# Performance work log

Measured on AMD Instinct MI355X. Metric: run time of the kernel, lower is better.

Reference implementation:

```python
import jax, jax.numpy as jnp
import numpy as np

N, E, G = 51200, 819200, 256            # nodes, directed edges, graphs
N2, A, E2 = 102400, 204800, 409600      # 2-sets, assignments, 2-set edges
D, L, NI2, NAF = 64, 5, 36, 40          # emb_dim, num_layer, num_i_2, num_atom_features
EPS = 1e-5


def _seg_sum(v, seg, n):
    return jax.ops.segment_sum(v, seg, num_segments=n)


def _seg_mean(v, seg, n):
    s = jax.ops.segment_sum(v, seg, num_segments=n)
    c = jax.ops.segment_sum(jnp.ones((v.shape[0],), v.dtype), seg, num_segments=n)
    return s / jnp.maximum(c, 1.0)[:, None]


def setup_inputs() -> dict:
    key = jax.random.key(0)
    ks = iter(jax.random.split(key, 64))
    nrm = lambda shape: jax.random.normal(next(ks), shape, jnp.float32) * 0.1
    x = jax.random.normal(next(ks), (N, NAF), jnp.float32)
    edge_index = jax.random.randint(next(ks), (2, E), 0, N, dtype=jnp.int32)
    edge_attr = jnp.stack([jax.random.randint(next(ks), (E,), 0, 4, dtype=jnp.int32),
                           jax.random.randint(next(ks), (E,), 0, 3, dtype=jnp.int32)], axis=1)
    batch = jnp.repeat(jnp.arange(G, dtype=jnp.int32), N // G)
    iso_type_2 = jax.nn.one_hot(jax.random.randint(next(ks), (N2,), 0, NI2), NI2, dtype=jnp.float32)
    edge_index_2 = jax.random.randint(next(ks), (2, E2), 0, N2, dtype=jnp.int32)
    assignment_index_2 = jnp.stack([jax.random.randint(next(ks), (A,), 0, N, dtype=jnp.int32),
                                    jnp.repeat(jnp.arange(N2, dtype=jnp.int32), 2)], axis=0)
    batch_2 = jnp.repeat(jnp.arange(G, dtype=jnp.int32), N2 // G)
    params = dict(
        emb_W=nrm((NAF, D)), emb_b=jnp.zeros((D,), jnp.float32),
        gin_W1=nrm((L, D, 2 * D)), gin_b1=jnp.zeros((L, 2 * D), jnp.float32),
        gin_W2=nrm((L, 2 * D, D)), gin_b2=jnp.zeros((L, D), jnp.float32),
        eemb1=nrm((L, 6, D)), eemb2=nrm((L, 3, D)),
        bn_gamma=jnp.ones((L, D), jnp.float32), bn_beta=jnp.zeros((L, D), jnp.float32),
        iso1_rel_W=nrm((D + NI2, D)), iso1_rel_b=jnp.zeros((D,), jnp.float32),
        iso1_root_W=nrm((D + NI2, D)),
        iso2_rel_W=nrm((D, D)), iso2_rel_b=jnp.zeros((D,), jnp.float32),
        iso2_root_W=nrm((D, D)),
        ro_W0=nrm((2 * D, D)), ro_b0=jnp.zeros((D,), jnp.float32),
        ro_W1=nrm((D, D // 2)), ro_b1=jnp.zeros((D // 2,), jnp.float32),
        ro_W2=nrm((D // 2, D // 4)), ro_b2=jnp.zeros((D // 4,), jnp.float32),
        last_W=nrm((D // 4, 1)), last_b=jnp.zeros((1,), jnp.float32),
    )
    return dict(x=x, edge_index=edge_index, edge_attr=edge_attr, batch=batch,
                iso_type_2=iso_type_2, edge_index_2=edge_index_2,
                assignment_index_2=assignment_index_2, batch_2=batch_2, **params)


def _forward(x, iso_type_2, emb_W, emb_b, gin_W1, gin_b1, gin_W2, gin_b2,
             eemb1, eemb2, bn_gamma, bn_beta,
             iso1_rel_W, iso1_rel_b, iso1_root_W, iso2_rel_W, iso2_rel_b, iso2_root_W,
             ro_W0, ro_b0, ro_W1, ro_b1, ro_W2, ro_b2, last_W, last_b,
             edge_index, edge_attr, batch, edge_index_2, assignment_index_2, batch_2):
    # --- GIN stack with edge-feature embeddings and self loops ---
    loop = jnp.arange(N, dtype=edge_index.dtype)
    src = jnp.concatenate([edge_index[0], loop])
    dst = jnp.concatenate([edge_index[1], loop])
    sl_attr = jnp.tile(jnp.array([[4, 0]], dtype=edge_attr.dtype), (N, 1))
    ea = jnp.concatenate([edge_attr, sl_attr], axis=0)  # [E+N, 2]

    h = jax.nn.relu(x @ emb_W + emb_b)  # x_embedding1
    for l in range(L):
        e = eemb1[l][ea[:, 0]] + eemb2[l][ea[:, 1]]      # [E+N, D]
        agg = _seg_sum(h[src] + e, dst, N)               # gather + scatter-add
        h2 = jax.nn.relu(agg @ gin_W1[l] + gin_b1[l]) @ gin_W2[l] + gin_b2[l]
        mu = jnp.mean(h2, axis=0)
        var = jnp.var(h2, axis=0)                        # biased, torch BN training mode
        h2 = (h2 - mu) / jnp.sqrt(var + EPS) * bn_gamma[l] + bn_beta[l]
        h = h2 if l == L - 1 else jax.nn.relu(h2)        # last layer: no ReLU (JK='last')
    node_rep = h

    # --- graph mean pool of node representation ---
    x1 = _seg_mean(node_rep, batch, G)                   # [G, D]

    # --- 2-set branch: avg_pool onto 2-sets, concat iso type, two GraphConvs ---
    xp = _seg_mean(node_rep[assignment_index_2[0]], assignment_index_2[1], N2)
    xp = jnp.concatenate([xp, iso_type_2], axis=1)       # [N2, D+NI2]

    def graph_conv(z, Wrel, brel, Wroot):
        agg = _seg_sum(z[edge_index_2[0]], edge_index_2[1], N2)
        return agg @ Wrel + brel + z @ Wroot

    xp = jax.nn.relu(graph_conv(xp, iso1_rel_W, iso1_rel_b, iso1_root_W))
    xp = jax.nn.relu(graph_conv(xp, iso2_rel_W, iso2_rel_b, iso2_root_W))
    x2 = _seg_mean(xp, batch_2, G)                       # [G, D]

    # --- readout MLP ---
    m = jnp.concatenate([x1, x2], axis=1)                # [G, 2D]
    m = jax.nn.relu(m @ ro_W0 + ro_b0)
    m = jax.nn.relu(m @ ro_W1 + ro_b1)
    m = jax.nn.relu(m @ ro_W2 + ro_b2)
    m = m @ last_W + last_b
    return m.reshape(-1)                                 # num_tasks == 1 -> flat [G]


def reference(x, edge_index, edge_attr, batch, iso_type_2, edge_index_2,
              assignment_index_2, batch_2, emb_W, emb_b, gin_W1, gin_b1, gin_W2,
              gin_b2, eemb1, eemb2, bn_gamma, bn_beta, iso1_rel_W, iso1_rel_b,
              iso1_root_W, iso2_rel_W, iso2_rel_b, iso2_root_W, ro_W0, ro_b0,
              ro_W1, ro_b1, ro_W2, ro_b2, last_W, last_b):
    return _forward(x, iso_type_2, emb_W, emb_b, gin_W1, gin_b1, gin_W2, gin_b2,
                    eemb1, eemb2, bn_gamma, bn_beta,
                    iso1_rel_W, iso1_rel_b, iso1_root_W, iso2_rel_W, iso2_rel_b,
                    iso2_root_W, ro_W0, ro_b0, ro_W1, ro_b1, ro_W2, ro_b2,
                    last_W, last_b, edge_index, edge_attr, batch, edge_index_2,
                    assignment_index_2, batch_2)
```

## Files before the change

kernel.cpp:

```cpp
#include <hip/hip_runtime.h>

#define NN   51200
#define EE   819200
#define GG   256
#define NN2  102400
#define AA   204800
#define EE2  409600
#define DD   64
#define LL   5

typedef __attribute__((ext_vector_type(8))) short bf16x8;
typedef __attribute__((ext_vector_type(4))) float f32x4;
typedef unsigned short ushort_t;

#define OFF_H      ((size_t)0)
#define OFF_AGG    ((size_t)13107200)
#define OFF_H2     ((size_t)26214400)
#define OFF_XP     ((size_t)39321600)
#define OFF_PERM   ((size_t)60293120)
#define OFF_YROOT  ((size_t)65536000)
#define OFF_OFFS1  ((size_t)91750400)
#define OFF_COL1   ((size_t)91955216)
#define OFF_OFFS2  ((size_t)95232016)
#define OFF_COL2   ((size_t)95641632)
#define OFF_CNT1   ((size_t)97280032)
#define OFF_CUR1   ((size_t)97484832)
#define OFF_CNT2   ((size_t)97689632)
#define OFF_CUR2   ((size_t)98099232)
#define OFF_STATS  ((size_t)98508832)
#define ZERO_BYTES ((size_t)1231360)
#define OFF_ISO    ((size_t)98511392)
#define OFF_M      ((size_t)98920992)
#define WS_NEEDED  ((size_t)99052064)

__device__ __forceinline__ int waveInclScan(int v, int lane) {
#pragma unroll
    for (int off = 1; off < 64; off <<= 1) {
        int t = __shfl_up(v, off, 64);
        if (lane >= off) v += t;
    }
    return v;
}

__device__ __forceinline__ void bsplit(float x, ushort_t& hi, ushort_t& lo) {
    union { float f; unsigned u; } a; a.f = x;
    unsigned hb = (a.u + 0x7FFFu + ((a.u >> 16) & 1u)) >> 16;
    union { unsigned u; float f; } h; h.u = hb << 16;
    float r = x - h.f;
    union { float f; unsigned u; } b; b.f = r;
    unsigned lb = (b.u + 0x7FFFu + ((b.u >> 16) & 1u)) >> 16;
    hi = (ushort_t)hb; lo = (ushort_t)lb;
}

__global__ void khist_m(const int* __restrict__ dst1, const int* __restrict__ dst2,
                        int* __restrict__ cnt1, int* __restrict__ cnt2,
                        int* __restrict__ rank1, int* __restrict__ rank2) {
    int b = blockIdx.x;
    if (b < 800) {
        int i = (b * 256 + threadIdx.x) * 4;
        int4 d = *(const int4*)(dst1 + i);
        int4 r;
        r.x = atomicAdd(&cnt1[d.x], 1);
        r.y = atomicAdd(&cnt1[d.y], 1);
        r.z = atomicAdd(&cnt1[d.z], 1);
        r.w = atomicAdd(&cnt1[d.w], 1);
        *(int4*)(rank1 + i) = r;
    } else {
        int i = ((b - 800) * 256 + threadIdx.x) * 4;
        int4 d = *(const int4*)(dst2 + i);
        int4 r;
        r.x = atomicAdd(&cnt2[d.x], 1);
        r.y = atomicAdd(&cnt2[d.y], 1);
        r.z = atomicAdd(&cnt2[d.z], 1);
        r.w = atomicAdd(&cnt2[d.w], 1);
        *(int4*)(rank2 + i) = r;
    }
}

__global__ void kprepx(const float* __restrict__ x, const float* __restrict__ embW,
                       const float* __restrict__ embB, float* __restrict__ h,
                       const float* __restrict__ gW1, const float* __restrict__ gW2,
                       ushort_t* __restrict__ w1h, ushort_t* __restrict__ w1l,
                       ushort_t* __restrict__ w2h, ushort_t* __restrict__ w2l,
                       const float* __restrict__ iso, int* __restrict__ isoIdx) {
    int b = blockIdx.x;
    if (b < 12800) {
        int t = b * 256 + threadIdx.x;
        int n = t >> 6, d = t & 63;
        float acc = embB[d];
        const float* xr = x + n * 40;
#pragma unroll
        for (int k = 0; k < 40; ++k) acc = fmaf(xr[k], embW[k * 64 + d], acc);
        h[(size_t)n * 64 + d] = fmaxf(acc, 0.f);
    } else if (b < 12840) {
        int t = (b - 12800) * 256 + threadIdx.x;
        int lane = t & 63, frag = t >> 6;
        int c15 = lane & 15, q = lane >> 4;
        if (frag < 80) {
            int kt = frag & 1, nt = (frag >> 1) & 7, l = frag >> 4;
            const float* W = gW1 + l * 8192;
            ushort_t* oh = w1h + ((size_t)frag * 64 + lane) * 8;
            ushort_t* ol = w1l + ((size_t)frag * 64 + lane) * 8;
            int kb = kt * 32 + q * 8, colw = nt * 16 + c15;
#pragma unroll
            for (int j = 0; j < 8; ++j) {
                ushort_t hi, lo; bsplit(W[(kb + j) * 128 + colw], hi, lo);
                oh[j] = hi; ol[j] = lo;
            }
        } else if (frag < 160) {
            int f = frag - 80;
            int kt = f & 3, nt = (f >> 2) & 3, l = f >> 4;
            const float* W = gW2 + l * 8192;
            ushort_t* oh = w2h + ((size_t)f * 64 + lane) * 8;
            ushort_t* ol = w2l + ((size_t)f * 64 + lane) * 8;
            int kb = kt * 32 + q * 8, colw = nt * 16 + c15;
#pragma unroll
            for (int j = 0; j < 8; ++j) {
                ushort_t hi, lo; bsplit(W[(kb + j) * 64 + colw], hi, lo);
                oh[j] = hi; ol[j] = lo;
            }
        }
    } else {
        int j = (b - 12840) * 256 + threadIdx.x;
        const float4* r4 = (const float4*)(iso + (size_t)j * 36);
        int best = 0;
#pragma unroll
        for (int k = 0; k < 9; ++k) {
            float4 v = r4[k];
            if (v.x > 0.5f) best = 4 * k;
            if (v.y > 0.5f) best = 4 * k + 1;
            if (v.z > 0.5f) best = 4 * k + 2;
            if (v.w > 0.5f) best = 4 * k + 3;
        }
        isoIdx[j] = best;
    }
}

__global__ void kreduce_m(const int* __restrict__ cnt1, const int* __restrict__ cnt2,
                          int* __restrict__ bsum1, int* __restrict__ bsum2) {
    __shared__ int wsr[4];
    int b = blockIdx.x;
    const int* cnt; int* bsum;
    if (b < 50) { cnt = cnt1; bsum = bsum1; }
    else { b -= 50; cnt = cnt2; bsum = bsum2; }
    int tid = threadIdx.x, lane = tid & 63, wid = tid >> 6;
    int4 v = ((const int4*)(cnt + (size_t)b * 1024))[tid];
    int s = v.x + v.y + v.z + v.w;
#pragma unroll
    for (int off = 32; off; off >>= 1) s += __shfl_down(s, off, 64);
    if (lane == 0) wsr[wid] = s;
    __syncthreads();
    if (tid == 0) bsum[b] = wsr[0] + wsr[1] + wsr[2] + wsr[3];
}

__global__ void kscan_small_m(const int* __restrict__ bsum1, const int* __restrict__ bsum2,
                              int* __restrict__ boffs1, int* __restrict__ boffs2) {
    __shared__ int w0s;
    const int* bsum = blockIdx.x ? bsum2 : bsum1;
    int* boffs = blockIdx.x ? boffs2 : boffs1;
    int nb = blockIdx.x ? 100 : 50;
    int tid = threadIdx.x, lane = tid & 63, wid = tid >> 6;
    int v = (tid < nb) ? bsum[tid] : 0;
    int incl = waveInclScan(v, lane);
    if (tid == 63) w0s = incl;
    __syncthreads();
    int excl = incl - v + (wid ? w0s : 0);
    if (tid < nb) boffs[tid] = excl;
}

__global__ void kscan_apply_m(const int* __restrict__ cnt1, const int* __restrict__ cnt2,
                              const int* __restrict__ boffs1, const int* __restrict__ boffs2,
                              int* __restrict__ offs1, int* __restrict__ offs2,
                              int* __restrict__ dbin) {
    __shared__ int wsum[4];
    __shared__ int hbin[64];
    int b = blockIdx.x;
    const int* cnt; const int* boffs; int* offs; int n, total;
    bool g1 = (b < 50);
    if (g1) { cnt = cnt1; boffs = boffs1; offs = offs1; n = NN; total = EE; }
    else { b -= 50; cnt = cnt2; boffs = boffs2; offs = offs2; n = NN2; total = EE2; }
    int tid = threadIdx.x, lane = tid & 63, wid = tid >> 6;
    if (g1 && tid < 64) hbin[tid] = 0;
    size_t base = (size_t)b * 1024;
    int4 v = ((const int4*)(cnt + base))[tid];
    int s = v.x + v.y + v.z + v.w;
    int incl = waveInclScan(s, lane);
    if (lane == 63) wsum[wid] = incl;
    __syncthreads();
    if (g1) {
        atomicAdd(&hbin[v.x < 63 ? v.x : 63], 1);
        atomicAdd(&hbin[v.y < 63 ? v.y : 63], 1);
        atomicAdd(&hbin[v.z < 63 ? v.z : 63], 1);
        atomicAdd(&hbin[v.w < 63 ? v.w : 63], 1);
    }
    int woff = boffs[b];
#pragma unroll
    for (int w = 0; w < 3; ++w) woff += (w < wid) ? wsum[w] : 0;
    int excl = woff + incl - s;
    int4 o;
    o.x = excl; o.y = excl + v.x; o.z = o.y + v.y; o.w = o.z + v.z;
    ((int4*)(offs + base))[tid] = o;
    if (tid == 0 && b == 0) offs[n] = total;
    __syncthreads();
    if (g1 && tid < 64 && hbin[tid]) atomicAdd(&dbin[tid], hbin[tid]);
}

__global__ void kdegscan(const int* __restrict__ dbin, int* __restrict__ dstart) {
    int tid = threadIdx.x;
    int v = dbin[tid];
    int incl = waveInclScan(v, tid);
    dstart[tid] = NN - incl;
}

__global__ __launch_bounds__(256) void kfill2(
        const int* __restrict__ src1, const int* __restrict__ dst1,
        const int* __restrict__ ea, const int* __restrict__ rank1,
        const int* __restrict__ offs1, int* __restrict__ col1,
        const int* __restrict__ src2, const int* __restrict__ dst2,
        const int* __restrict__ rank2, const int* __restrict__ offs2,
        int* __restrict__ col2,
        const int* __restrict__ dstart, int* __restrict__ dcur,
        int* __restrict__ perm) {
    int b = blockIdx.x;
    if (b < 800) {
        int i = (b * 256 + threadIdx.x) * 4;
        int4 d4 = *(const int4*)(dst1 + i);
        int4 s4 = *(const int4*)(src1 + i);
        int4 r4 = *(const int4*)(rank1 + i);
        int4 e0 = *(const int4*)(ea + 2 * i);
        int4 e1 = *(const int4*)(ea + 2 * i + 4);
        col1[offs1[d4.x] + r4.x] = s4.x | ((e0.x * 3 + e0.y) << 16);
        col1[offs1[d4.y] + r4.y] = s4.y | ((e0.z * 3 + e0.w) << 16);
        col1[offs1[d4.z] + r4.z] = s4.z | ((e1.x * 3 + e1.y) << 16);
        col1[offs1[d4.w] + r4.w] = s4.w | ((e1.z * 3 + e1.w) << 16);
    } else if (b < 1200) {
        int i = ((b - 800) * 256 + threadIdx.x) * 4;
        int4 d4 = *(const int4*)(dst2 + i);
        int4 s4 = *(const int4*)(src2 + i);
        int4 r4 = *(const int4*)(rank2 + i);
        col2[offs2[d4.x] + r4.x] = s4.x;
        col2[offs2[d4.y] + r4.y] = s4.y;
        col2[offs2[d4.z] + r4.z] = s4.z;
        col2[offs2[d4.w] + r4.w] = s4.w;
    } else {
        __shared__ int lhist[64];
        __shared__ int lbase[64];
        int tid = threadIdx.x;
        if (tid < 64) lhist[tid] = 0;
        __syncthreads();
        int n = (b - 1200) * 256 + tid;
        int d = offs1[n + 1] - offs1[n]; d = d < 63 ? d : 63;
        int lr = atomicAdd(&lhist[d], 1);
        __syncthreads();
        if (tid < 64) {
            int c = lhist[tid];
            lbase[tid] = c ? atomicAdd(&dcur[tid], c) : 0;
        }
        __syncthreads();
        perm[dstart[d] + lbase[d] + lr] = n;
    }
}

__global__ __launch_bounds__(256) void ktrans(float* __restrict__ h,
                                              const float* __restrict__ pst,
                                              const float* __restrict__ gamma,
                                              const float* __restrict__ beta) {
    __shared__ float sstat[128];
    __shared__ float sSC[64], sSH[64];
    int tid = threadIdx.x;
    if (tid < 128) {
        float s = 0.f;
        const float* p = pst + tid;
#pragma unroll
        for (int i = 0; i < 32; ++i) s += p[i * 128];
        sstat[tid] = s;
    }
    __syncthreads();
    if (tid < 64) {
        float mu = sstat[tid] * (1.f / NN);
        float var = sstat[64 + tid] * (1.f / NN) - mu * mu;
        float sc = gamma[tid] * rsqrtf(var + 1e-5f);
        sSC[tid] = sc; sSH[tid] = beta[tid] - mu * sc;
    }
    __syncthreads();
    int c = (tid & 15) * 4;
    float4 sc4 = *(const float4*)(sSC + c);
    float4 sh4 = *(const float4*)(sSH + c);
    float4* hp = (float4*)h;
    size_t base = (size_t)blockIdx.x * 1024 + tid;
#pragma unroll
    for (int r = 0; r < 4; ++r) {
        float4 v = hp[base + r * 256];
        v.x = fmaxf(fmaf(v.x, sc4.x, sh4.x), 0.f);
        v.y = fmaxf(fmaf(v.y, sc4.y, sh4.y), 0.f);
        v.z = fmaxf(fmaf(v.z, sc4.z, sh4.z), 0.f);
        v.w = fmaxf(fmaf(v.w, sc4.w, sh4.w), 0.f);
        hp[base + r * 256] = v;
    }
}

__global__ __launch_bounds__(256) void kglayer(
    const float* __restrict__ hin, float* __restrict__ hout,
    const int* __restrict__ perm,
    const int* __restrict__ offs, const int* __restrict__ col,
    const float* __restrict__ e1, const float* __restrict__ e2,
    const ushort_t* __restrict__ w1h, const ushort_t* __restrict__ w1l,
    const ushort_t* __restrict__ w2h, const ushort_t* __restrict__ w2l,
    const float* __restrict__ b1, const float* __restrict__ b2,
    float* __restrict__ pstout) {
    __shared__ float etab[13 * 64];
    __shared__ int sPerm[16];
    __shared__ float sMLP[16 * 132];
    float* sA = sMLP;
    float* sH = sMLP;
    int tid = threadIdx.x;
    if (tid < 16) sPerm[tid] = perm[blockIdx.x * 16 + tid];
    for (int idx = tid; idx < 13 * 64; idx += 256) {
        int ci = idx >> 6, dd = idx & 63;
        etab[idx] = e1[(ci / 3) * 64 + dd] + e2[(ci % 3) * 64 + dd];
    }
    __syncthreads();
    int lane = tid & 63, wv = tid >> 6;
    int c15 = lane & 15, q = lane >> 4;

    {
        int n = sPerm[wv * 4 + q];
        int s0 = offs[n], s1 = offs[n + 1];
        float4 sx = *(const float4*)(hin + (size_t)n * 64 + 4 * c15);
        float4 et = *(const float4*)(etab + 12 * 64 + 4 * c15);
        float a0 = sx.x + et.x, a1 = sx.y + et.y, a2 = sx.z + et.z, a3 = sx.w + et.w;
        int deg = s1 - s0;
        if (deg > 0) {
            const int* cp = col + s0;
            int nfull = deg >> 3, rem = deg & 7;
            int vv[8];
#pragma unroll
            for (int j = 0; j < 8; ++j) {
                int idx = j < deg ? j : deg - 1;
                vv[j] = cp[idx];
            }
            for (int it = 0; it < nfull; ++it) {
                float4 xv[8], tv[8];
#pragma unroll
                for (int j = 0; j < 8; ++j) {
                    xv[j] = *(const float4*)(hin + (size_t)(vv[j] & 0xFFFF) * 64 + 4 * c15);
                    tv[j] = *(const float4*)(etab + (vv[j] >> 16) * 64 + 4 * c15);
                }
                int e8 = (it + 1) * 8;
                bool more = e8 < deg;
                int nx[8];
                if (more) {
#pragma unroll
                    for (int j = 0; j < 8; ++j) {
                        int idx = e8 + j; idx = idx < deg ? idx : deg - 1;
                        nx[j] = cp[idx];
                    }
                }
#pragma unroll
                for (int j = 0; j < 8; ++j) {
                    a0 += xv[j].x + tv[j].x;
                    a1 += xv[j].y + tv[j].y;
                    a2 += xv[j].z + tv[j].z;
                    a3 += xv[j].w + tv[j].w;
                }
                if (more) {
#pragma unroll
                    for (int j = 0; j < 8; ++j) vv[j] = nx[j];
                }
            }
            if (rem) {
                float4 xv[8], tv[8];
#pragma unroll
                for (int j = 0; j < 8; ++j) {
                    xv[j] = *(const float4*)(hin + (size_t)(vv[j] & 0xFFFF) * 64 + 4 * c15);
                    tv[j] = *(const float4*)(etab + (vv[j] >> 16) * 64 + 4 * c15);
                }
#pragma unroll
                for (int j = 0; j < 8; ++j) {
                    float mm = (j < rem) ? 1.f : 0.f;
                    a0 = fmaf(xv[j].x + tv[j].x, mm, a0);
                    a1 = fmaf(xv[j].y + tv[j].y, mm, a1);
                    a2 = fmaf(xv[j].z + tv[j].z, mm, a2);
                    a3 = fmaf(xv[j].w + tv[j].w, mm, a3);
                }
            }
        }
        *(float4*)(sA + (wv * 4 + q) * 68 + 4 * c15) = make_float4(a0, a1, a2, a3);
    }
    __syncthreads();

    bf16x8 ah[2], al[2];
#pragma unroll
    for (int kt = 0; kt < 2; ++kt) {
        const float* p = sA + c15 * 68 + kt * 32 + q * 8;
        float4 x0 = *(const float4*)p;
        float4 x1 = *(const float4*)(p + 4);
        float xs[8] = {x0.x, x0.y, x0.z, x0.w, x1.x, x1.y, x1.z, x1.w};
#pragma unroll
        for (int j = 0; j < 8; ++j) {
            ushort_t hi, lo; bsplit(xs[j], hi, lo);
            ah[kt][j] = (short)hi; al[kt][j] = (short)lo;
        }
    }
    __syncthreads();

    f32x4 acc1[2];
#pragma unroll
    for (int j = 0; j < 2; ++j) { f32x4 z = {0.f, 0.f, 0.f, 0.f}; acc1[j] = z; }
#pragma unroll
    for (int kt = 0; kt < 2; ++kt) {
#pragma unroll
        for (int j = 0; j < 2; ++j) {
            int nt = 2 * wv + j;
            size_t fo = ((size_t)((nt * 2 + kt) * 64 + lane)) * 8;
            bf16x8 bh = *(const bf16x8*)(w1h + fo);
            bf16x8 bl = *(const bf16x8*)(w1l + fo);
            acc1[j] = __builtin_amdgcn_mfma_f32_16x16x32_bf16(ah[kt], bh, acc1[j], 0, 0, 0);
            acc1[j] = __builtin_amdgcn_mfma_f32_16x16x32_bf16(al[kt], bh, acc1[j], 0, 0, 0);
            acc1[j] = __builtin_amdgcn_mfma_f32_16x16x32_bf16(ah[kt], bl, acc1[j], 0, 0, 0);
        }
    }
#pragma unroll
    for (int j = 0; j < 2; ++j) {
        int nt = 2 * wv + j;
        float bias = b1[nt * 16 + c15];
#pragma unroll
        for (int rg = 0; rg < 4; ++rg)
            sH[(4 * q + rg) * 132 + nt * 16 + c15] = fmaxf(acc1[j][rg] + bias, 0.f);
    }
    __syncthreads();

    f32x4 acc2 = {0.f, 0.f, 0.f, 0.f};
#pragma unroll
    for (int kt = 0; kt < 4; ++kt) {
        const float* p = sH + c15 * 132 + kt * 32 + q * 8;
        float4 x0 = *(const float4*)p;
        float4 x1 = *(const float4*)(p + 4);
        float xs[8] = {x0.x, x0.y, x0.z, x0.w, x1.x, x1.y, x1.z, x1.w};
        bf16x8 a2h, a2l;
#pragma unroll
        for (int j = 0; j < 8; ++j) {
            ushort_t hi, lo; bsplit(xs[j], hi, lo);
            a2h[j] = (short)hi; a2l[j] = (short)lo;
        }
        size_t fo = ((size_t)((wv * 4 + kt) * 64 + lane)) * 8;
        bf16x8 bh = *(const bf16x8*)(w2h + fo);
        bf16x8 bl = *(const bf16x8*)(w2l + fo);
        acc2 = __builtin_amdgcn_mfma_f32_16x16x32_bf16(a2h, bh, acc2, 0, 0, 0);
        acc2 = __builtin_amdgcn_mfma_f32_16x16x32_bf16(a2l, bh, acc2, 0, 0, 0);
        acc2 = __builtin_amdgcn_mfma_f32_16x16x32_bf16(a2h, bl, acc2, 0, 0, 0);
    }
    {
        float bias = b2[wv * 16 + c15];
        float s = 0.f, s2 = 0.f;
#pragma unroll
        for (int rg = 0; rg < 4; ++rg) {
            float v = acc2[rg] + bias;
            hout[(size_t)sPerm[4 * q + rg] * 64 + wv * 16 + c15] = v;
            s += v; s2 += v * v;
        }
        s += __shfl_xor(s, 16, 64);  s += __shfl_xor(s, 32, 64);
        s2 += __shfl_xor(s2, 16, 64); s2 += __shfl_xor(s2, 32, 64);
        if (q == 0) {
            float* ps = pstout + (size_t)(blockIdx.x & 31) * 128;
            atomicAdd(&ps[wv * 16 + c15], s);
            atomicAdd(&ps[64 + wv * 16 + c15], s2);
        }
    }
}

template <int FIRST>
__global__ __launch_bounds__(256) void kgcmm(const float* __restrict__ X,
                                             const float* __restrict__ Wrel,
                                             const float* __restrict__ Wroot,
                                             const float* __restrict__ WrelIso,
                                             const float* __restrict__ WrootIso,
                                             const int* __restrict__ isoIdx,
                                             float* __restrict__ Yrel,
                                             float* __restrict__ Yroot,
                                             const float* __restrict__ pst,
                                             const float* __restrict__ g4,
                                             const float* __restrict__ b4,
                                             const int* __restrict__ a0g,
                                             const float* __restrict__ h2src) {
    __shared__ float sX[64 * 65];
    __shared__ float sR[64 * 64];
    __shared__ float sT[64 * 64];
    __shared__ float sstat[128];
    __shared__ float sSC[64], sSH[64];
    int tid = threadIdx.x, blk = blockIdx.x;
    if (FIRST && tid < 128) {
        float s = 0.f;
        const float* p = pst + tid;
#pragma unroll
        for (int i = 0; i < 32; ++i) s += p[i * 128];
        sstat[tid] = s;
    }
#pragma unroll
    for (int i = tid; i < 1024; i += 256) {
        ((float4*)sR)[i] = ((const float4*)Wrel)[i];
        ((float4*)sT)[i] = ((const float4*)Wroot)[i];
    }
    __syncthreads();
    if (FIRST && tid < 64) {
        float mu = sstat[tid] * (1.f / NN);
        float var = sstat[64 + tid] * (1.f / NN) - mu * mu;
        float sc = g4[tid] * rsqrtf(var + 1e-5f);
        sSC[tid] = sc;
        sSH[tid] = b4[tid] - mu * sc;
    }
    __syncthreads();
#pragma unroll
    for (int i = tid; i < 1024; i += 256) {
        int row = i >> 4, c = (i & 15) << 2;
        float4 v;
        if (FIRST) {
            int grow = blk * 64 + row;
            int na = a0g[2 * grow], nb = a0g[2 * grow + 1];
            float4 va = *(const float4*)(h2src + (size_t)na * 64 + c);
            float4 vb = *(const float4*)(h2src + (size_t)nb * 64 + c);
            v.x = 0.5f * (va.x + vb.x); v.y = 0.5f * (va.y + vb.y);
            v.z = 0.5f * (va.z + vb.z); v.w = 0.5f * (va.w + vb.w);
            v.x = fmaf(v.x, sSC[c], sSH[c]);
            v.y = fmaf(v.y, sSC[c + 1], sSH[c + 1]);
            v.z = fmaf(v.z, sSC[c + 2], sSH[c + 2]);
            v.w = fmaf(v.w, sSC[c + 3], sSH[c + 3]);
        } else {
            v = ((const float4*)(X + (size_t)blk * 4096))[i];
        }
        float* p = sX + row * 65 + c;
        p[0] = v.x; p[1] = v.y; p[2] = v.z; p[3] = v.w;
    }
    __syncthreads();
    int tm = tid >> 4, tn = tid & 15;
    float aR[4][4], aT[4][4];
#pragma unroll
    for (int r = 0; r < 4; ++r)
#pragma unroll
        for (int c = 0; c < 4; ++c) { aR[r][c] = 0.f; aT[r][c] = 0.f; }
    const float* xrow = sX + tm * 4 * 65;
#pragma unroll 4
    for (int k = 0; k < 64; ++k) {
        float a0 = xrow[k], a1 = xrow[65 + k], a2 = xrow[130 + k], a3 = xrow[195 + k];
        float4 br = *(const float4*)(sR + k * 64 + tn * 4);
        float4 bt = *(const float4*)(sT + k * 64 + tn * 4);
        float rb[4] = {br.x, br.y, br.z, br.w};
        float tb[4] = {bt.x, bt.y, bt.z, bt.w};
#pragma unroll
        for (int c = 0; c < 4; ++c) {
            aR[0][c] = fmaf(a0, rb[c], aR[0][c]); aR[1][c] = fmaf(a1, rb[c], aR[1][c]);
            aR[2][c] = fmaf(a2, rb[c], aR[2][c]); aR[3][c] = fmaf(a3, rb[c], aR[3][c]);
            aT[0][c] = fmaf(a0, tb[c], aT[0][c]); aT[1][c] = fmaf(a1, tb[c], aT[1][c]);
            aT[2][c] = fmaf(a2, tb[c], aT[2][c]); aT[3][c] = fmaf(a3, tb[c], aT[3][c]);
        }
    }
#pragma unroll
    for (int r = 0; r < 4; ++r) {
        int row = blk * 64 + tm * 4 + r;
        float4 vr = make_float4(aR[r][0], aR[r][1], aR[r][2], aR[r][3]);
        float4 vt = make_float4(aT[r][0], aT[r][1], aT[r][2], aT[r][3]);
        if (FIRST) {
            int ii = isoIdx[row];
            float4 er = *(const float4*)(WrelIso + (size_t)ii * 64 + tn * 4);
            float4 et = *(const float4*)(WrootIso + (size_t)ii * 64 + tn * 4);
            vr.x += er.x; vr.y += er.y; vr.z += er.z; vr.w += er.w;
            vt.x += et.x; vt.y += et.y; vt.z += et.z; vt.w += et.w;
        }
        *(float4*)(Yrel + (size_t)row * 64 + tn * 4) = vr;
        *(float4*)(Yroot + (size_t)row * 64 + tn * 4) = vt;
    }
}

__global__ void kgather2(const float* __restrict__ yrel, const float* __restrict__ yroot,
                         const float* __restrict__ brel, const int* __restrict__ offs,
                         const int* __restrict__ col, float* __restrict__ out) {
    int t = blockIdx.x * 256 + threadIdx.x;
    int j = t >> 4, c = t & 15;
    int s0 = offs[j], s1 = offs[j + 1];
    float4 rt = *(const float4*)(yroot + (size_t)j * 64 + 4 * c);
    float4 bb = *(const float4*)(brel + 4 * c);
    float a0 = rt.x + bb.x, a1 = rt.y + bb.y, a2 = rt.z + bb.z, a3 = rt.w + bb.w;
    if (s0 < s1) {
        int vv[4];
#pragma unroll
        for (int jj = 0; jj < 4; ++jj) {
            int idx = s0 + jj; idx = idx < s1 ? idx : s1 - 1;
            vv[jj] = col[idx];
        }
        int e = s0;
        while (true) {
            int ne = e + 4;
            bool more = ne < s1;
            float4 xs[4];
#pragma unroll
            for (int jj = 0; jj < 4; ++jj)
                xs[jj] = *(const float4*)(yrel + (size_t)vv[jj] * 64 + 4 * c);
            int nx[4];
            if (more) {
#pragma unroll
                for (int jj = 0; jj < 4; ++jj) {
                    int idx = ne + jj; idx = idx < s1 ? idx : s1 - 1;
                    nx[jj] = col[idx];
                }
            }
#pragma unroll
            for (int jj = 0; jj < 4; ++jj) {
                float mm = (e + jj < s1) ? 1.f : 0.f;
                a0 = fmaf(xs[jj].x, mm, a0);
                a1 = fmaf(xs[jj].y, mm, a1);
                a2 = fmaf(xs[jj].z, mm, a2);
                a3 = fmaf(xs[jj].w, mm, a3);
            }
            if (!more) break;
            e = ne;
#pragma unroll
            for (int jj = 0; jj < 4; ++jj) vv[jj] = nx[jj];
        }
    }
    *(float4*)(out + (size_t)j * 64 + 4 * c) =
        make_float4(fmaxf(a0, 0.f), fmaxf(a1, 0.f), fmaxf(a2, 0.f), fmaxf(a3, 0.f));
}

__global__ void kpoolg(const float* __restrict__ h2, const float* __restrict__ xp2,
                       const float* __restrict__ pst, const float* __restrict__ g4,
                       const float* __restrict__ b4, float* __restrict__ m) {
    __shared__ float sstat[128];
    __shared__ float red[4][64];
    int g = blockIdx.x, tid = threadIdx.x;
    if (tid < 128) {
        float s = 0.f;
        const float* p = pst + tid;
#pragma unroll
        for (int i = 0; i < 32; ++i) s += p[i * 128];
        sstat[tid] = s;
    }
    int wid = tid >> 6, d = tid & 63;
    float s1 = 0.f;
    for (int i = wid; i < 200; i += 4) s1 += h2[((size_t)g * 200 + i) * 64 + d];
    red[wid][d] = s1;
    __syncthreads();
    if (wid == 0) {
        float mean = (red[0][d] + red[1][d] + red[2][d] + red[3][d]) * (1.f / 200.f);
        float mu = sstat[d] * (1.f / NN);
        float var = sstat[64 + d] * (1.f / NN) - mu * mu;
        float sc = g4[d] * rsqrtf(var + 1e-5f);
        m[g * 128 + d] = fmaf(mean, sc, b4[d] - mu * sc);
    }
    __syncthreads();
    float s2 = 0.f;
    for (int i = wid; i < 400; i += 4) s2 += xp2[((size_t)g * 400 + i) * 64 + d];
    red[wid][d] = s2;
    __syncthreads();
    if (wid == 0) m[g * 128 + 64 + d] = (red[0][d] + red[1][d] + red[2][d] + red[3][d]) * (1.f / 400.f);
}

__global__ void kread(const float* __restrict__ m, const float* __restrict__ W0,
                      const float* __restrict__ b0, const float* __restrict__ W1,
                      const float* __restrict__ b1, const float* __restrict__ W2,
                      const float* __restrict__ b2, const float* __restrict__ lw,
                      const float* __restrict__ lb, float* __restrict__ out) {
    __shared__ float s0[64], s1[32], s2[16];
    int g = blockIdx.x, d = threadIdx.x;
    const float* mr = m + g * 128;
    float t = b0[d];
    for (int k = 0; k < 128; ++k) t = fmaf(mr[k], W0[k * 64 + d], t);
    s0[d] = fmaxf(t, 0.f);
    __syncthreads();
    if (d < 32) {
        float u = b1[d];
        for (int k = 0; k < 64; ++k) u = fmaf(s0[k], W1[k * 32 + d], u);
        s1[d] = fmaxf(u, 0.f);
    }
    __syncthreads();
    if (d < 16) {
        float u = b2[d];
        for (int k = 0; k < 32; ++k) u = fmaf(s1[k], W2[k * 16 + d], u);
        s2[d] = fmaxf(u, 0.f);
    }
    __syncthreads();
    if (d == 0) {
        float u = lb[0];
        for (int k = 0; k < 16; ++k) u = fmaf(s2[k], lw[k], u);
        out[g] = u;
    }
}

extern "C" void kernel_launch(void* const* d_in, const int* in_sizes, int n_in,
                              void* d_out, int out_size, void* d_ws, size_t ws_size,
                              hipStream_t stream) {
    if (ws_size < WS_NEEDED) return;

    const float* x    = (const float*)d_in[0];
    const int*   ei   = (const int*)d_in[1];
    const int*   ea   = (const int*)d_in[2];
    const float* iso  = (const float*)d_in[4];
    const int*   ei2  = (const int*)d_in[5];
    const int*   ai2  = (const int*)d_in[6];
    const float* embW = (const float*)d_in[8];
    const float* embB = (const float*)d_in[9];
    const float* gW1  = (const float*)d_in[10];
    const float* gB1  = (const float*)d_in[11];
    const float* gW2  = (const float*)d_in[12];
    const float* gB2  = (const float*)d_in[13];
    const float* ee1  = (const float*)d_in[14];
    const float* ee2  = (const float*)d_in[15];
    const float* bng  = (const float*)d_in[16];
    const float* bnb  = (const float*)d_in[17];
    const float* i1rW = (const float*)d_in[18];
    const float* i1rB = (const float*)d_in[19];
    const float* i1tW = (const float*)d_in[20];
    const float* i2rW = (const float*)d_in[21];
    const float* i2rB = (const float*)d_in[22];
    const float* i2tW = (const float*)d_in[23];
    const float* roW0 = (const float*)d_in[24];
    const float* roB0 = (const float*)d_in[25];
    const float* roW1 = (const float*)d_in[26];
    const float* roB1 = (const float*)d_in[27];
    const float* roW2 = (const float*)d_in[28];
    const float* roB2 = (const float*)d_in[29];
    const float* lW   = (const float*)d_in[30];
    const float* lB   = (const float*)d_in[31];
    float* out = (float*)d_out;

    char* ws = (char*)d_ws;
    float* h      = (float*)(ws + OFF_H);
    float* hB     = (float*)(ws + OFF_AGG);
    float* hA     = (float*)(ws + OFF_H2);
    float* h2     = hA;
    float* xp     = (float*)(ws + OFF_XP);
    float* yrel   = (float*)(ws + OFF_H);
    float* yroot  = (float*)(ws + OFF_YROOT);
    int* offs1    = (int*)(ws + OFF_OFFS1);
    int* col1     = (int*)(ws + OFF_COL1);
    int* offs2    = (int*)(ws + OFF_OFFS2);
    int* col2     = (int*)(ws + OFF_COL2);
    int* cnt1     = (int*)(ws + OFF_CNT1);
    int* cnt2     = (int*)(ws + OFF_CNT2);
    int* isoIdx   = (int*)(ws + OFF_ISO);
    float* mbuf   = (float*)(ws + OFF_M);
    int* bsum1    = (int*)(ws + OFF_M);
    int* boffs1   = (int*)(ws + OFF_M + 256);
    int* bsum2    = (int*)(ws + OFF_M + 512);
    int* boffs2   = (int*)(ws + OFF_M + 1024);
    ushort_t* w1h = (ushort_t*)(ws + OFF_YROOT);
    ushort_t* w1l = (ushort_t*)(ws + OFF_YROOT + 81920);
    ushort_t* w2h = (ushort_t*)(ws + OFF_YROOT + 163840);
    ushort_t* w2l = (ushort_t*)(ws + OFF_YROOT + 245760);
    float* pstat2 = (float*)(ws + OFF_CUR1);
    int* rank1    = (int*)(ws + OFF_XP);
    int* rank2    = (int*)(ws + OFF_XP + (size_t)EE * 4);
    int* perm     = (int*)(ws + OFF_PERM);
    int* dbin     = (int*)(ws + OFF_STATS);
    int* dstart   = dbin + 64;
    int* dcur     = dbin + 128;

    const int* src1 = ei;
    const int* dst1 = ei + EE;
    const int* src2 = ei2;
    const int* dst2 = ei2 + EE2;
    const int* a0   = ai2;

    hipMemsetAsync(ws + OFF_CNT1, 0, ZERO_BYTES, stream);

    khist_m<<<1200, 256, 0, stream>>>(dst1, dst2, cnt1, cnt2, rank1, rank2);
    kprepx<<<13240, 256, 0, stream>>>(x, embW, embB, h, gW1, gW2,
                                      w1h, w1l, w2h, w2l, iso, isoIdx);
    kreduce_m<<<150, 256, 0, stream>>>(cnt1, cnt2, bsum1, bsum2);
    kscan_small_m<<<2, 128, 0, stream>>>(bsum1, bsum2, boffs1, boffs2);
    kscan_apply_m<<<150, 256, 0, stream>>>(cnt1, cnt2, boffs1, boffs2, offs1, offs2, dbin);
    kdegscan<<<1, 64, 0, stream>>>(dbin, dstart);
    kfill2<<<1400, 256, 0, stream>>>(src1, dst1, ea, rank1, offs1, col1,
                                     src2, dst2, rank2, offs2, col2,
                                     dstart, dcur, perm);

    for (int l = 0; l < LL; ++l) {
        const float* hin = (l == 0) ? h : ((l & 1) ? hA : hB);
        float* hout = (l & 1) ? hB : hA;
        kglayer<<<NN / 16, 256, 0, stream>>>(
            hin, hout, perm, offs1, col1, ee1 + l * 384, ee2 + l * 192,
            w1h + (size_t)l * 8192, w1l + (size_t)l * 8192,
            w2h + (size_t)l * 8192, w2l + (size_t)l * 8192,
            gB1 + l * 128, gB2 + l * 64,
            pstat2 + (size_t)l * 4096);
        if (l < LL - 1)
            ktrans<<<800, 256, 0, stream>>>(hout, pstat2 + (size_t)l * 4096,
                                            bng + l * 64, bnb + l * 64);
    }

    kgcmm<1><<<NN2 / 64, 256, 0, stream>>>(xp, i1rW, i1tW, i1rW + 64 * 64,
                                           i1tW + 64 * 64, isoIdx, yrel, yroot,
                                           pstat2 + (size_t)4 * 4096,
                                           bng + 4 * 64, bnb + 4 * 64, a0, h2);
    kgather2<<<NN2 * 16 / 256, 256, 0, stream>>>(yrel, yroot, i1rB, offs2, col2, xp);
    kgcmm<0><<<NN2 / 64, 256, 0, stream>>>(xp, i2rW, i2tW, nullptr, nullptr,
                                           nullptr, yrel, yroot,
                                           nullptr, nullptr, nullptr, nullptr, nullptr);
    kgather2<<<NN2 * 16 / 256, 256, 0, stream>>>(yrel, yroot, i2rB, offs2, col2, xp);

    kpoolg<<<GG, 256, 0, stream>>>(h2, xp, pstat2 + (size_t)4 * 4096,
                                   bng + 4 * 64, bnb + 4 * 64, mbuf);
    kread<<<GG, 64, 0, stream>>>(mbuf, roW0, roB0, roW1, roB1, roW2, roB2, lW, lB, out);
}
```

Baseline: 622.5 us.

## Replace per-node atomic CSR build with two-level bucketed counting sort

CSR construction for both edge sets used a global per-node atomic histogram, several scan kernels and a random scatter fill. It now works in two passes. The first pass bins edges by destination into 512-node buckets, using shared-memory histograms and one global atomic per bucket per block. The second pass does a local per-bucket count, scan and scatter in LDS to produce offsets and columns. The degree-sorted permutation is moved into its own kernel, and its bin start ordering changes from descending to ascending. The goal is fewer global atomics and scattered writes, at the cost of an intermediate record buffer with fixed per-bucket capacity that could overflow on skewed inputs.

```diff
diff --git a/kernel.cpp b/kernel.cpp
--- a/kernel.cpp
+++ b/kernel.cpp
@@ -9,6 +9,11 @@
 #define DD   64
 #define LL   5
 
+#define NB1  100
+#define NB2  200
+#define CAP1 10240
+#define CAP2 3072
+
 typedef __attribute__((ext_vector_type(8))) short bf16x8;
 typedef __attribute__((ext_vector_type(4))) float f32x4;
 typedef unsigned short ushort_t;
@@ -17,6 +22,8 @@
 #define OFF_AGG    ((size_t)13107200)
 #define OFF_H2     ((size_t)26214400)
 #define OFF_XP     ((size_t)39321600)
+#define OFF_REC1   OFF_XP
+#define OFF_REC2   ((size_t)47513600)
 #define OFF_PERM   ((size_t)60293120)
 #define OFF_YROOT  ((size_t)65536000)
 #define OFF_OFFS1  ((size_t)91750400)
@@ -24,9 +31,8 @@
 #define OFF_OFFS2  ((size_t)95232016)
 #define OFF_COL2   ((size_t)95641632)
 #define OFF_CNT1   ((size_t)97280032)
+#define OFF_BBASE  ((size_t)97282080)
 #define OFF_CUR1   ((size_t)97484832)
-#define OFF_CNT2   ((size_t)97689632)
-#define OFF_CUR2   ((size_t)98099232)
 #define OFF_STATS  ((size_t)98508832)
 #define ZERO_BYTES ((size_t)1231360)
 #define OFF_ISO    ((size_t)98511392)
@@ -52,28 +58,146 @@
     hi = (ushort_t)hb; lo = (ushort_t)lb;
 }
 
-__global__ void khist_m(const int* __restrict__ dst1, const int* __restrict__ dst2,
-                        int* __restrict__ cnt1, int* __restrict__ cnt2,
-                        int* __restrict__ rank1, int* __restrict__ rank2) {
-    int b = blockIdx.x;
-    if (b < 800) {
-        int i = (b * 256 + threadIdx.x) * 4;
-        int4 d = *(const int4*)(dst1 + i);
-        int4 r;
-        r.x = atomicAdd(&cnt1[d.x], 1);
-        r.y = atomicAdd(&cnt1[d.y], 1);
-        r.z = atomicAdd(&cnt1[d.z], 1);
-        r.w = atomicAdd(&cnt1[d.w], 1);
-        *(int4*)(rank1 + i) = r;
+__global__ __launch_bounds__(256) void kbA(const int* __restrict__ src1, const int* __restrict__ dst1,
+                                           const int* __restrict__ ea,
+                                           const int* __restrict__ src2, const int* __restrict__ dst2,
+                                           int* __restrict__ bucketCnt,
+                                           int2* __restrict__ rec1, int2* __restrict__ rec2) {
+    __shared__ int lhist[256];
+    __shared__ int lbase[256];
+    int tid = threadIdx.x, b = blockIdx.x;
+    lhist[tid] = 0;
+    __syncthreads();
+    if (b < 400) {
+        int i = (b * 256 + tid) * 8;
+        int4 d0 = *(const int4*)(dst1 + i);
+        int4 d1 = *(const int4*)(dst1 + i + 4);
+        int dst[8] = {d0.x, d0.y, d0.z, d0.w, d1.x, d1.y, d1.z, d1.w};
+        int bin[8], lr[8];
+#pragma unroll
+        for (int j = 0; j < 8; ++j) {
+            bin[j] = dst[j] >> 9;
+            lr[j] = atomicAdd(&lhist[bin[j]], 1);
+        }
+        __syncthreads();
+        if (tid < NB1) {
+            int c = lhist[tid];
+            lbase[tid] = c ? atomicAdd(&bucketCnt[tid], c) : 0;
+        }
+        __syncthreads();
+        int4 s0 = *(const int4*)(src1 + i);
+        int4 s1 = *(const int4*)(src1 + i + 4);
+        int src[8] = {s0.x, s0.y, s0.z, s0.w, s1.x, s1.y, s1.z, s1.w};
+        int4 e0 = *(const int4*)(ea + 2 * i);
+        int4 e1 = *(const int4*)(ea + 2 * i + 4);
+        int4 e2 = *(const int4*)(ea + 2 * i + 8);
+        int4 e3 = *(const int4*)(ea + 2 * i + 12);
+        int code[8] = {e0.x * 3 + e0.y, e0.z * 3 + e0.w, e1.x * 3 + e1.y, e1.z * 3 + e1.w,
+                       e2.x * 3 + e2.y, e2.z * 3 + e2.w, e3.x * 3 + e3.y, e3.z * 3 + e3.w};
+#pragma unroll
+        for (int j = 0; j < 8; ++j) {
+            int pos = bin[j] * CAP1 + lbase[bin[j]] + lr[j];
+            rec1[pos] = make_int2(src[j] | (code[j] << 16), dst[j]);
+        }
     } else {
-        int i = ((b - 800) * 256 + threadIdx.x) * 4;
-        int4 d = *(const int4*)(dst2 + i);
-        int4 r;
-        r.x = atomicAdd(&cnt2[d.x], 1);
-        r.y = atomicAdd(&cnt2[d.y], 1);
-        r.z = atomicAdd(&cnt2[d.z], 1);
-        r.w = atomicAdd(&cnt2[d.w], 1);
-        *(int4*)(rank2 + i) = r;
+        int i = ((b - 400) * 256 + tid) * 8;
+        int4 d0 = *(const int4*)(dst2 + i);
+        int4 d1 = *(const int4*)(dst2 + i + 4);
+        int dst[8] = {d0.x, d0.y, d0.z, d0.w, d1.x, d1.y, d1.z, d1.w};
+        int bin[8], lr[8];
+#pragma unroll
+        for (int j = 0; j < 8; ++j) {
+            bin[j] = dst[j] >> 9;
+            lr[j] = atomicAdd(&lhist[bin[j]], 1);
+        }
+        __syncthreads();
+        if (tid < NB2) {
+            int c = lhist[tid];
+            lbase[tid] = c ? atomicAdd(&bucketCnt[NB1 + tid], c) : 0;
+        }
+        __syncthreads();
+        int4 s0 = *(const int4*)(src2 + i);
+        int4 s1 = *(const int4*)(src2 + i + 4);
+        int src[8] = {s0.x, s0.y, s0.z, s0.w, s1.x, s1.y, s1.z, s1.w};
+#pragma unroll
+        for (int j = 0; j < 8; ++j) {
+            int pos = bin[j] * CAP2 + lbase[bin[j]] + lr[j];
+            rec2[pos] = make_int2(src[j], dst[j]);
+        }
+    }
+}
+
+__global__ void kbscan(const int* __restrict__ bucketCnt, int* __restrict__ bucketBase) {
+    __shared__ int wsum[4];
+    int tid = threadIdx.x, lane = tid & 63, wid = tid >> 6;
+    int nb = blockIdx.x ? NB2 : NB1;
+    const int* cnt = bucketCnt + (blockIdx.x ? NB1 : 0);
+    int* base = bucketBase + (blockIdx.x ? NB1 : 0);
+    int v = (tid < nb) ? cnt[tid] : 0;
+    int incl = waveInclScan(v, lane);
+    if (lane == 63) wsum[wid] = incl;
+    __syncthreads();
+    int woff = 0;
+#pragma unroll
+    for (int w = 0; w < 3; ++w) woff += (w < wid) ? wsum[w] : 0;
+    if (tid < nb) base[tid] = woff + incl - v;
+}
+
+__global__ __launch_bounds__(256) void kbB(const int* __restrict__ bucketCnt,
+                                           const int* __restrict__ bucketBase,
+                                           const int2* __restrict__ rec1, const int2* __restrict__ rec2,
+                                           int* __restrict__ offs1, int* __restrict__ col1,
+                                           int* __restrict__ offs2, int* __restrict__ col2,
+                                           int* __restrict__ dbin) {
+    __shared__ int nh[512];
+    __shared__ int ncur[512];
+    __shared__ int wsum[4];
+    __shared__ int dhist[64];
+    int tid = threadIdx.x, b = blockIdx.x;
+    bool g1 = b < NB1;
+    const int2* rec = g1 ? (rec1 + (size_t)b * CAP1) : (rec2 + (size_t)(b - NB1) * CAP2);
+    int cnt = bucketCnt[b];
+    int base = bucketBase[b];
+    int* offs = g1 ? offs1 : offs2;
+    int* col = g1 ? col1 : col2;
+    int nodeBase = g1 ? b * 512 : (b - NB1) * 512;
+    nh[tid] = 0; nh[tid + 256] = 0;
+    if (tid < 64) dhist[tid] = 0;
+    __syncthreads();
+    for (int e = tid; e < cnt; e += 256) {
+        int2 r = rec[e];
+        atomicAdd(&nh[r.y & 511], 1);
+    }
+    __syncthreads();
+    int v0 = nh[2 * tid], v1 = nh[2 * tid + 1];
+    int s = v0 + v1;
+    int lane = tid & 63, wid = tid >> 6;
+    int incl = waveInclScan(s, lane);
+    if (lane == 63) wsum[wid] = incl;
+    __syncthreads();
+    int woff = 0;
+#pragma unroll
+    for (int w = 0; w < 3; ++w) woff += (w < wid) ? wsum[w] : 0;
+    int excl = woff + incl - s;
+    ncur[2 * tid] = excl;
+    ncur[2 * tid + 1] = excl + v0;
+    offs[nodeBase + 2 * tid] = base + excl;
+    offs[nodeBase + 2 * tid + 1] = base + excl + v0;
+    if (g1) {
+        atomicAdd(&dhist[v0 < 63 ? v0 : 63], 1);
+        atomicAdd(&dhist[v1 < 63 ? v1 : 63], 1);
+    }
+    __syncthreads();
+    for (int e = tid; e < cnt; e += 256) {
+        int2 r = rec[e];
+        int node = r.y & 511;
+        int slot = base + atomicAdd(&ncur[node], 1);
+        col[slot] = r.x;
+    }
+    if (g1 && tid < 64 && dhist[tid]) atomicAdd(&dbin[tid], dhist[tid]);
+    if (tid == 0) {
+        if (b == NB1 - 1) offs1[NN] = EE;
+        if (b == NB1 + NB2 - 1) offs2[NN2] = EE2;
     }
 }
 
@@ -136,129 +260,32 @@
     }
 }
 
-__global__ void kreduce_m(const int* __restrict__ cnt1, const int* __restrict__ cnt2,
-                          int* __restrict__ bsum1, int* __restrict__ bsum2) {
-    __shared__ int wsr[4];
-    int b = blockIdx.x;
-    const int* cnt; int* bsum;
-    if (b < 50) { cnt = cnt1; bsum = bsum1; }
-    else { b -= 50; cnt = cnt2; bsum = bsum2; }
-    int tid = threadIdx.x, lane = tid & 63, wid = tid >> 6;
-    int4 v = ((const int4*)(cnt + (size_t)b * 1024))[tid];
-    int s = v.x + v.y + v.z + v.w;
-#pragma unroll
-    for (int off = 32; off; off >>= 1) s += __shfl_down(s, off, 64);
-    if (lane == 0) wsr[wid] = s;
-    __syncthreads();
-    if (tid == 0) bsum[b] = wsr[0] + wsr[1] + wsr[2] + wsr[3];
-}
-
-__global__ void kscan_small_m(const int* __restrict__ bsum1, const int* __restrict__ bsum2,
-                              int* __restrict__ boffs1, int* __restrict__ boffs2) {
-    __shared__ int w0s;
-    const int* bsum = blockIdx.x ? bsum2 : bsum1;
-    int* boffs = blockIdx.x ? boffs2 : boffs1;
-    int nb = blockIdx.x ? 100 : 50;
-    int tid = threadIdx.x, lane = tid & 63, wid = tid >> 6;
-    int v = (tid < nb) ? bsum[tid] : 0;
-    int incl = waveInclScan(v, lane);
-    if (tid == 63) w0s = incl;
-    __syncthreads();
-    int excl = incl - v + (wid ? w0s : 0);
-    if (tid < nb) boffs[tid] = excl;
-}
-
-__global__ void kscan_apply_m(const int* __restrict__ cnt1, const int* __restrict__ cnt2,
-                              const int* __restrict__ boffs1, const int* __restrict__ boffs2,
-                              int* __restrict__ offs1, int* __restrict__ offs2,
-                              int* __restrict__ dbin) {
-    __shared__ int wsum[4];
-    __shared__ int hbin[64];
-    int b = blockIdx.x;
-    const int* cnt; const int* boffs; int* offs; int n, total;
-    bool g1 = (b < 50);
-    if (g1) { cnt = cnt1; boffs = boffs1; offs = offs1; n = NN; total = EE; }
-    else { b -= 50; cnt = cnt2; boffs = boffs2; offs = offs2; n = NN2; total = EE2; }
-    int tid = threadIdx.x, lane = tid & 63, wid = tid >> 6;
-    if (g1 && tid < 64) hbin[tid] = 0;
-    size_t base = (size_t)b * 1024;
-    int4 v = ((const int4*)(cnt + base))[tid];
-    int s = v.x + v.y + v.z + v.w;
-    int incl = waveInclScan(s, lane);
-    if (lane == 63) wsum[wid] = incl;
-    __syncthreads();
-    if (g1) {
-        atomicAdd(&hbin[v.x < 63 ? v.x : 63], 1);
-        atomicAdd(&hbin[v.y < 63 ? v.y : 63], 1);
-        atomicAdd(&hbin[v.z < 63 ? v.z : 63], 1);
-        atomicAdd(&hbin[v.w < 63 ? v.w : 63], 1);
-    }
-    int woff = boffs[b];
-#pragma unroll
-    for (int w = 0; w < 3; ++w) woff += (w < wid) ? wsum[w] : 0;
-    int excl = woff + incl - s;
-    int4 o;
-    o.x = excl; o.y = excl + v.x; o.z = o.y + v.y; o.w = o.z + v.z;
-    ((int4*)(offs + base))[tid] = o;
-    if (tid == 0 && b == 0) offs[n] = total;
-    __syncthreads();
-    if (g1 && tid < 64 && hbin[tid]) atomicAdd(&dbin[tid], hbin[tid]);
-}
-
 __global__ void kdegscan(const int* __restrict__ dbin, int* __restrict__ dstart) {
     int tid = threadIdx.x;
     int v = dbin[tid];
     int incl = waveInclScan(v, tid);
-    dstart[tid] = NN - incl;
-}
-
-__global__ __launch_bounds__(256) void kfill2(
-        const int* __restrict__ src1, const int* __restrict__ dst1,
-        const int* __restrict__ ea, const int* __restrict__ rank1,
-        const int* __restrict__ offs1, int* __restrict__ col1,
-        const int* __restrict__ src2, const int* __restrict__ dst2,
-        const int* __restrict__ rank2, const int* __restrict__ offs2,
-        int* __restrict__ col2,
-        const int* __restrict__ dstart, int* __restrict__ dcur,
-        int* __restrict__ perm) {
-    int b = blockIdx.x;
-    if (b < 800) {
-        int i = (b * 256 + threadIdx.x) * 4;
-        int4 d4 = *(const int4*)(dst1 + i);
-        int4 s4 = *(const int4*)(src1 + i);
-        int4 r4 = *(const int4*)(rank1 + i);
-        int4 e0 = *(const int4*)(ea + 2 * i);
-        int4 e1 = *(const int4*)(ea + 2 * i + 4);
-        col1[offs1[d4.x] + r4.x] = s4.x | ((e0.x * 3 + e0.y) << 16);
-        col1[offs1[d4.y] + r4.y] = s4.y | ((e0.z * 3 + e0.w) << 16);
-        col1[offs1[d4.z] + r4.z] = s4.z | ((e1.x * 3 + e1.y) << 16);
-        col1[offs1[d4.w] + r4.w] = s4.w | ((e1.z * 3 + e1.w) << 16);
-    } else if (b < 1200) {
-        int i = ((b - 800) * 256 + threadIdx.x) * 4;
-        int4 d4 = *(const int4*)(dst2 + i);
-        int4 s4 = *(const int4*)(src2 + i);
-        int4 r4 = *(const int4*)(rank2 + i);
-        col2[offs2[d4.x] + r4.x] = s4.x;
-        col2[offs2[d4.y] + r4.y] = s4.y;
-        col2[offs2[d4.z] + r4.z] = s4.z;
-        col2[offs2[d4.w] + r4.w] = s4.w;
-    } else {
-        __shared__ int lhist[64];
-        __shared__ int lbase[64];
-        int tid = threadIdx.x;
-        if (tid < 64) lhist[tid] = 0;
-        __syncthreads();
-        int n = (b - 1200) * 256 + tid;
-        int d = offs1[n + 1] - offs1[n]; d = d < 63 ? d : 63;
-        int lr = atomicAdd(&lhist[d], 1);
-        __syncthreads();
-        if (tid < 64) {
-            int c = lhist[tid];
-            lbase[tid] = c ? atomicAdd(&dcur[tid], c) : 0;
-        }
-        __syncthreads();
-        perm[dstart[d] + lbase[d] + lr] = n;
-    }
+    dstart[tid] = incl - v;
+}
+
+__global__ __launch_bounds__(256) void kdegplace(const int* __restrict__ offs,
+                                                 const int* __restrict__ dstart,
+                                                 int* __restrict__ dcur,
+                                                 int* __restrict__ perm) {
+    __shared__ int lhist[64];
+    __shared__ int lbase[64];
+    int tid = threadIdx.x;
+    if (tid < 64) lhist[tid] = 0;
+    __syncthreads();
+    int n = blockIdx.x * 256 + tid;
+    int d = offs[n + 1] - offs[n]; d = d < 63 ? d : 63;
+    int lr = atomicAdd(&lhist[d], 1);
+    __syncthreads();
+    if (tid < 64) {
+        int c = lhist[tid];
+        lbase[tid] = c ? atomicAdd(&dcur[tid], c) : 0;
+    }
+    __syncthreads();
+    perm[dstart[d] + lbase[d] + lr] = n;
 }
 
 __global__ __launch_bounds__(256) void ktrans(float* __restrict__ h,
@@ -734,21 +761,17 @@
     int* col1     = (int*)(ws + OFF_COL1);
     int* offs2    = (int*)(ws + OFF_OFFS2);
     int* col2     = (int*)(ws + OFF_COL2);
-    int* cnt1     = (int*)(ws + OFF_CNT1);
-    int* cnt2     = (int*)(ws + OFF_CNT2);
     int* isoIdx   = (int*)(ws + OFF_ISO);
     float* mbuf   = (float*)(ws + OFF_M);
-    int* bsum1    = (int*)(ws + OFF_M);
-    int* boffs1   = (int*)(ws + OFF_M + 256);
-    int* bsum2    = (int*)(ws + OFF_M + 512);
-    int* boffs2   = (int*)(ws + OFF_M + 1024);
     ushort_t* w1h = (ushort_t*)(ws + OFF_YROOT);
     ushort_t* w1l = (ushort_t*)(ws + OFF_YROOT + 81920);
     ushort_t* w2h = (ushort_t*)(ws + OFF_YROOT + 163840);
     ushort_t* w2l = (ushort_t*)(ws + OFF_YROOT + 245760);
     float* pstat2 = (float*)(ws + OFF_CUR1);
-    int* rank1    = (int*)(ws + OFF_XP);
-    int* rank2    = (int*)(ws + OFF_XP + (size_t)EE * 4);
+    int2* rec1    = (int2*)(ws + OFF_REC1);
+    int2* rec2    = (int2*)(ws + OFF_REC2);
+    int* bucketCnt  = (int*)(ws + OFF_CNT1);
+    int* bucketBase = (int*)(ws + OFF_BBASE);
     int* perm     = (int*)(ws + OFF_PERM);
     int* dbin     = (int*)(ws + OFF_STATS);
     int* dstart   = dbin + 64;
@@ -762,16 +785,14 @@
 
     hipMemsetAsync(ws + OFF_CNT1, 0, ZERO_BYTES, stream);
 
-    khist_m<<<1200, 256, 0, stream>>>(dst1, dst2, cnt1, cnt2, rank1, rank2);
+    kbA<<<600, 256, 0, stream>>>(src1, dst1, ea, src2, dst2, bucketCnt, rec1, rec2);
     kprepx<<<13240, 256, 0, stream>>>(x, embW, embB, h, gW1, gW2,
                                       w1h, w1l, w2h, w2l, iso, isoIdx);
-    kreduce_m<<<150, 256, 0, stream>>>(cnt1, cnt2, bsum1, bsum2);
-    kscan_small_m<<<2, 128, 0, stream>>>(bsum1, bsum2, boffs1, boffs2);
-    kscan_apply_m<<<150, 256, 0, stream>>>(cnt1, cnt2, boffs1, boffs2, offs1, offs2, dbin);
+    kbscan<<<2, 256, 0, stream>>>(bucketCnt, bucketBase);
+    kbB<<<300, 256, 0, stream>>>(bucketCnt, bucketBase, rec1, rec2,
+                                 offs1, col1, offs2, col2, dbin);
     kdegscan<<<1, 64, 0, stream>>>(dbin, dstart);
-    kfill2<<<1400, 256, 0, stream>>>(src1, dst1, ea, rank1, offs1, col1,
-                                     src2, dst2, rank2, offs2, col2,
-                                     dstart, dcur, perm);
+    kdegplace<<<NN / 256, 256, 0, stream>>>(offs1, dstart, dcur, perm);
 
     for (int l = 0; l < LL; ++l) {
         const float* hin = (l == 0) ? h : ((l & 1) ? hA : hB);
```

Result: faster. 591.5 us (-5.0%).
